# Kernel tuning notes

Hardware: AMD Instinct MI355X
Metric: run time of the kernel (lower is better)

## Reference

```python
import jax, jax.numpy as jnp
import numpy as np

B, IN, OUT = 131072, 128, 32
GRID_SIZE, SPLINE_ORDER = 5, 3
GRID_LO, GRID_HI = -1.0, 1.0
N_BASIS = GRID_SIZE + SPLINE_ORDER  # 8


def _centers_and_spacing():
    n_knots = GRID_SIZE + 2 * SPLINE_ORDER + 1  # 12
    grid = jnp.linspace(GRID_LO, GRID_HI, n_knots)
    centers = grid[SPLINE_ORDER:SPLINE_ORDER + N_BASIS]  # (8,)
    spacing = (GRID_HI - GRID_LO) / GRID_SIZE + 1e-06
    return centers, spacing


def setup_inputs() -> dict:
    key = jax.random.key(0)
    k1, k2, k3 = jax.random.split(key, 3)
    x = jax.random.normal(k1, (B, IN), dtype=jnp.float32)
    coeff = jax.random.normal(k2, (IN, OUT, N_BASIS), dtype=jnp.float32) * 0.1
    base_weight = jnp.ones((IN, OUT), dtype=jnp.float32)
    base_bias = jnp.zeros((IN, OUT), dtype=jnp.float32)
    edge_weights = jax.random.normal(k3, (IN, OUT), dtype=jnp.float32) * 0.1
    return {"x": x, "coeff": coeff, "base_weight": base_weight,
            "base_bias": base_bias, "edge_weights": edge_weights}


def reference(x, coeff, base_weight, base_bias, edge_weights):
    # y[b,j] = sum_i w[i,j] * ( bw[i,j]*silu(x[b,i]) + bb[i,j]
    #                           + sum_k basis[b,i,k]*coeff[i,j,k] )
    centers, spacing = _centers_and_spacing()
    silu = x * jax.nn.sigmoid(x)                                    # (B, I)
    z = (x[:, :, None] - centers[None, None, :]) / spacing          # (B, I, K)
    basis = jnp.exp(-0.5 * z * z)                                   # (B, I, K)
    # base activation contribution
    base_out = jnp.einsum('bi,ij->bj', silu, edge_weights * base_weight)
    bias_out = jnp.sum(edge_weights * base_bias, axis=0)            # (J,)
    # spline contribution: contract over input dim i and basis dim k
    spline_out = jnp.einsum('bik,ijk->bj', basis,
                            edge_weights[:, :, None] * coeff)
    return base_out + bias_out[None, :] + spline_out
```

## Files before the change

### kernel.cpp

```cpp
#include <hip/hip_runtime.h>

typedef short bf16x8 __attribute__((ext_vector_type(8)));
typedef float f32x4v __attribute__((ext_vector_type(4)));

constexpr double H_D    = 0.4 + 1e-6;
constexpr double INVH_D = 1.0 / H_D;
constexpr double C0_D   = -1.0 + 6.0 / 11.0;
constexpr double DLT_D  = (2.0 / 11.0) / H_D;
constexpr double L2E_D  = 1.4426950408889634;

constexpr float INVH = (float)INVH_D;
constexpr float NC0H = (float)(-C0_D * INVH_D);
constexpr float A2f  = (float)(-0.5 * L2E_D);
constexpr float B2f  = (float)(DLT_D * L2E_D);
constexpr float GCF  = (float)(-0.5 * DLT_D * DLT_D * L2E_D);
constexpr float NL2E = (float)(-L2E_D);

__device__ __forceinline__ float fexp2(float v) {
#if __has_builtin(__builtin_amdgcn_exp2f)
  return __builtin_amdgcn_exp2f(v);
#else
  return exp2f(v);
#endif
}
__device__ __forceinline__ float frcp(float v) {
#if __has_builtin(__builtin_amdgcn_rcpf)
  return __builtin_amdgcn_rcpf(v);
#else
  return 1.0f / v;
#endif
}
__device__ __forceinline__ float siluf(float v) {
  return v * frcp(1.0f + fexp2(NL2E * v));
}
__device__ __forceinline__ unsigned pk2(float lo, float hi) {
  unsigned a = __float_as_uint(hi) + 0x8000u;
  unsigned b = __float_as_uint(lo) + 0x8000u;
  return __builtin_amdgcn_perm(a, b, 0x07060302u);
}
__device__ __forceinline__ bf16x8 packfrag(const float (&v)[8]) {
  uint4 d;
  d.x = pk2(v[0], v[1]);
  d.y = pk2(v[2], v[3]);
  d.z = pk2(v[4], v[5]);
  d.w = pk2(v[6], v[7]);
  return __builtin_bit_cast(bf16x8, d);
}
__device__ __forceinline__ unsigned rne16(float f) {
  unsigned u = __float_as_uint(f);
  return (u + 0x7fffu + ((u >> 16) & 1u)) >> 16;
}

__global__ void kan_prep(const float* __restrict__ coeff,
                         const float* __restrict__ bw,
                         const float* __restrict__ bb,
                         const float* __restrict__ ew,
                         uint4* __restrict__ wfrag,
                         float* __restrict__ bias) {
  if (blockIdx.x == 18) {
    __shared__ float part[256];
    const int n = threadIdx.x & 31;
    const int c = threadIdx.x >> 5;
    float s = 0.f;
#pragma unroll
    for (int i = c * 16; i < c * 16 + 16; ++i)
      s += ew[i * 32 + n] * bb[i * 32 + n];
    part[threadIdx.x] = s;
    __syncthreads();
    if (threadIdx.x < 32) {
      float t = 0.f;
#pragma unroll
      for (int c2 = 0; c2 < 8; ++c2) t += part[c2 * 32 + threadIdx.x];
      bias[threadIdx.x] = t;
    }
    return;
  }
  const int e    = blockIdx.x * 4 + (threadIdx.x >> 6);
  const int lane = threadIdx.x & 63;
  const int s = e >> 1, h = e & 1;
  const int G = s / 9, t = s % 9;
  const int n = h * 16 + (lane & 15);
  const int cbase = G * 32 + (lane >> 4) * 8;
  float v[8];
  if (t == 0) {
#pragma unroll
    for (int j = 0; j < 8; ++j) {
      int i = cbase + j;
      v[j] = ew[i * 32 + n] * bw[i * 32 + n];
    }
  } else {
    const int k = t - 1;
    const float g = exp2f(GCF * (float)(k * k));
#pragma unroll
    for (int j = 0; j < 8; ++j) {
      int i = cbase + j;
      v[j] = ew[i * 32 + n] * coeff[(i * 32 + n) * 8 + k] * g;
    }
  }
  uint4 d;
  d.x = (rne16(v[1]) << 16) | rne16(v[0]);
  d.y = (rne16(v[3]) << 16) | rne16(v[2]);
  d.z = (rne16(v[5]) << 16) | rne16(v[4]);
  d.w = (rne16(v[7]) << 16) | rne16(v[6]);
  wfrag[e * 64 + lane] = d;
}

__device__ __forceinline__ void gl_lds16(const uint4* g, uint4* l) {
  __builtin_amdgcn_global_load_lds(
      (const __attribute__((address_space(1))) void*)g,
      (__attribute__((address_space(3))) void*)l, 16, 0, 0);
}

__global__ __launch_bounds__(256, 8) void kan_main(
    const float* __restrict__ x,
    const uint4* __restrict__ wfrag,
    const float* __restrict__ bias,
    float* __restrict__ out) {
  __shared__ uint4 wlds[1152];
  const int tid  = threadIdx.x;
  const int lane = tid & 63;
  const int wave = tid >> 6;
  const int m    = lane & 15;
  const int quad = lane >> 4;
  const long rowbase = ((long)blockIdx.x * 4 + wave) * 16;

  f32x4v acc0, acc1;
#pragma unroll
  for (int rr = 0; rr < 4; ++rr) { acc0[rr] = 0.f; acc1[rr] = 0.f; }

  const float* xbase = x + (rowbase + m) * 128 + (long)quad * 8;

  float xb[8];
  {
    const float4* p = reinterpret_cast<const float4*>(xbase);
    float4 a = p[0], b = p[1];
    xb[0] = a.x; xb[1] = a.y; xb[2] = a.z; xb[3] = a.w;
    xb[4] = b.x; xb[5] = b.y; xb[6] = b.z; xb[7] = b.w;
  }
  const float bv0 = bias[m];
  const float bv1 = bias[m + 16];

#pragma unroll 1
  for (int G = 0; G < 4; ++G) {
    if (G) __syncthreads();
    const uint4* src = wfrag + (size_t)G * 1152;
#pragma unroll
    for (int i = 0; i < 4; ++i)
      gl_lds16(src + tid + i * 256, &wlds[tid + i * 256]);
    if (tid < 128) gl_lds16(src + 1024 + tid, &wlds[1024 + tid]);
    __syncthreads();

    bf16x8 af0;
    float pg[8], rg[8];
    {
      float sv[8];
#pragma unroll
      for (int j = 0; j < 8; ++j) sv[j] = siluf(xb[j]);
      af0 = packfrag(sv);
#pragma unroll
      for (int j = 0; j < 8; ++j) {
        float u = fmaf(xb[j], INVH, NC0H);
        pg[j] = fexp2(A2f * u * u);
        rg[j] = fexp2(B2f * u);
      }
    }

    if (G < 3) {
      const float4* p = reinterpret_cast<const float4*>(xbase + (G + 1) * 32);
      float4 a = p[0], b = p[1];
      xb[0] = a.x; xb[1] = a.y; xb[2] = a.z; xb[3] = a.w;
      xb[4] = b.x; xb[5] = b.y; xb[6] = b.z; xb[7] = b.w;
    }

    const uint4* wl = wlds + lane;

    acc0 = __builtin_amdgcn_mfma_f32_16x16x32_bf16(
        af0, __builtin_bit_cast(bf16x8, wl[0]), acc0, 0, 0, 0);
    acc1 = __builtin_amdgcn_mfma_f32_16x16x32_bf16(
        af0, __builtin_bit_cast(bf16x8, wl[64]), acc1, 0, 0, 0);

#pragma unroll
    for (int t = 1; t <= 8; ++t) {
      bf16x8 c0 = __builtin_bit_cast(bf16x8, wl[t * 128]);
      bf16x8 c1 = __builtin_bit_cast(bf16x8, wl[t * 128 + 64]);
      bf16x8 af = packfrag(pg);
      acc0 = __builtin_amdgcn_mfma_f32_16x16x32_bf16(af, c0, acc0, 0, 0, 0);
      acc1 = __builtin_amdgcn_mfma_f32_16x16x32_bf16(af, c1, acc1, 0, 0, 0);
      if (t < 8) {
#pragma unroll
        for (int j = 0; j < 8; ++j) pg[j] *= rg[j];
      }
    }
  }

#pragma unroll
  for (int rr = 0; rr < 4; ++rr) {
    long row = rowbase + quad * 4 + rr;
    out[row * 32 + m]      = acc0[rr] + bv0;
    out[row * 32 + m + 16] = acc1[rr] + bv1;
  }
}

extern "C" void kernel_launch(void* const* d_in, const int* in_sizes, int n_in,
                              void* d_out, int out_size, void* d_ws, size_t ws_size,
                              hipStream_t stream) {
  const float* x     = (const float*)d_in[0];
  const float* coeff = (const float*)d_in[1];
  const float* bw    = (const float*)d_in[2];
  const float* bb    = (const float*)d_in[3];
  const float* ew    = (const float*)d_in[4];

  uint4* wfrag = (uint4*)d_ws;
  float* bias  = (float*)((char*)d_ws + 73728);

  kan_prep<<<19, 256, 0, stream>>>(coeff, bw, bb, ew, wfrag, bias);
  kan_main<<<2048, 256, 0, stream>>>(x, wfrag, bias, (float*)d_out);
}
```

Before: 117.6 us.

## Double-buffer weight LDS, process two row tiles per wave, use hardware bf16 pack

Each wave now handles 32 rows instead of 16, so every LDS weight fragment read feeds two MFMAs and the grid is halved. The weight slices are double-buffered in LDS, with the next group's global-to-LDS copy issued before the current group's compute, which removes one barrier-bound load stall per group. The manual bf16 rounding trick is replaced by the v_cvt_pk_bf16_f32 instruction. The cost is higher register and LDS use per block, which is why the launch bound drops to 4 blocks per CU and lowers occupancy.

```diff
diff --git a/kernel.cpp b/kernel.cpp
--- a/kernel.cpp
+++ b/kernel.cpp
@@ -33,17 +33,17 @@
 __device__ __forceinline__ float siluf(float v) {
   return v * frcp(1.0f + fexp2(NL2E * v));
 }
-__device__ __forceinline__ unsigned pk2(float lo, float hi) {
-  unsigned a = __float_as_uint(hi) + 0x8000u;
-  unsigned b = __float_as_uint(lo) + 0x8000u;
-  return __builtin_amdgcn_perm(a, b, 0x07060302u);
+__device__ __forceinline__ unsigned pkbf(float lo, float hi) {
+  unsigned r;
+  asm("v_cvt_pk_bf16_f32 %0, %1, %2" : "=v"(r) : "v"(lo), "v"(hi));
+  return r;
 }
 __device__ __forceinline__ bf16x8 packfrag(const float (&v)[8]) {
   uint4 d;
-  d.x = pk2(v[0], v[1]);
-  d.y = pk2(v[2], v[3]);
-  d.z = pk2(v[4], v[5]);
-  d.w = pk2(v[6], v[7]);
+  d.x = pkbf(v[0], v[1]);
+  d.y = pkbf(v[2], v[3]);
+  d.z = pkbf(v[4], v[5]);
+  d.w = pkbf(v[6], v[7]);
   return __builtin_bit_cast(bf16x8, d);
 }
 __device__ __forceinline__ unsigned rne16(float f) {
@@ -111,93 +111,125 @@
       (__attribute__((address_space(3))) void*)l, 16, 0, 0);
 }
 
-__global__ __launch_bounds__(256, 8) void kan_main(
+__device__ __forceinline__ void ld8(const float* p, float (&v)[8]) {
+  const float4* q = reinterpret_cast<const float4*>(p);
+  float4 a = q[0], b = q[1];
+  v[0] = a.x; v[1] = a.y; v[2] = a.z; v[3] = a.w;
+  v[4] = b.x; v[5] = b.y; v[6] = b.z; v[7] = b.w;
+}
+
+__global__ __launch_bounds__(256, 4) void kan_main(
     const float* __restrict__ x,
     const uint4* __restrict__ wfrag,
     const float* __restrict__ bias,
     float* __restrict__ out) {
-  __shared__ uint4 wlds[1152];
+  __shared__ uint4 wlds[2][1152];
   const int tid  = threadIdx.x;
   const int lane = tid & 63;
   const int wave = tid >> 6;
   const int m    = lane & 15;
   const int quad = lane >> 4;
-  const long rowbase = ((long)blockIdx.x * 4 + wave) * 16;
-
-  f32x4v acc0, acc1;
-#pragma unroll
-  for (int rr = 0; rr < 4; ++rr) { acc0[rr] = 0.f; acc1[rr] = 0.f; }
-
-  const float* xbase = x + (rowbase + m) * 128 + (long)quad * 8;
-
-  float xb[8];
-  {
-    const float4* p = reinterpret_cast<const float4*>(xbase);
-    float4 a = p[0], b = p[1];
-    xb[0] = a.x; xb[1] = a.y; xb[2] = a.z; xb[3] = a.w;
-    xb[4] = b.x; xb[5] = b.y; xb[6] = b.z; xb[7] = b.w;
-  }
+  const long rowbase = ((long)blockIdx.x * 4 + wave) * 32;
+
+  f32x4v a0A, a1A, a0B, a1B;
+#pragma unroll
+  for (int rr = 0; rr < 4; ++rr) {
+    a0A[rr] = 0.f; a1A[rr] = 0.f; a0B[rr] = 0.f; a1B[rr] = 0.f;
+  }
+
+  const float* xpA = x + (rowbase + m) * 128 + (long)quad * 8;
+  const float* xpB = xpA + 16 * 128;
+
+  float xa[8], xb[8];
+  ld8(xpA, xa);
+  ld8(xpB, xb);
   const float bv0 = bias[m];
   const float bv1 = bias[m + 16];
 
+  {
+#pragma unroll
+    for (int i = 0; i < 4; ++i)
+      gl_lds16(wfrag + tid + i * 256, &wlds[0][tid + i * 256]);
+    if (tid < 128) gl_lds16(wfrag + 1024 + tid, &wlds[0][1024 + tid]);
+  }
+  __syncthreads();
+
 #pragma unroll 1
   for (int G = 0; G < 4; ++G) {
-    if (G) __syncthreads();
-    const uint4* src = wfrag + (size_t)G * 1152;
-#pragma unroll
-    for (int i = 0; i < 4; ++i)
-      gl_lds16(src + tid + i * 256, &wlds[tid + i * 256]);
-    if (tid < 128) gl_lds16(src + 1024 + tid, &wlds[1024 + tid]);
-    __syncthreads();
-
-    bf16x8 af0;
-    float pg[8], rg[8];
+    if (G < 3) {
+      const uint4* src = wfrag + (size_t)(G + 1) * 1152;
+      uint4* dst = &wlds[(G + 1) & 1][0];
+#pragma unroll
+      for (int i = 0; i < 4; ++i)
+        gl_lds16(src + tid + i * 256, dst + tid + i * 256);
+      if (tid < 128) gl_lds16(src + 1024 + tid, dst + 1024 + tid);
+    }
+
+    bf16x8 sA, sB;
+    float pA[8], rA[8], pB[8], rB[8];
     {
       float sv[8];
 #pragma unroll
+      for (int j = 0; j < 8; ++j) sv[j] = siluf(xa[j]);
+      sA = packfrag(sv);
+#pragma unroll
       for (int j = 0; j < 8; ++j) sv[j] = siluf(xb[j]);
-      af0 = packfrag(sv);
+      sB = packfrag(sv);
+#pragma unroll
+      for (int j = 0; j < 8; ++j) {
+        float u = fmaf(xa[j], INVH, NC0H);
+        pA[j] = fexp2(A2f * u * u);
+        rA[j] = fexp2(B2f * u);
+      }
 #pragma unroll
       for (int j = 0; j < 8; ++j) {
         float u = fmaf(xb[j], INVH, NC0H);
-        pg[j] = fexp2(A2f * u * u);
-        rg[j] = fexp2(B2f * u);
+        pB[j] = fexp2(A2f * u * u);
+        rB[j] = fexp2(B2f * u);
       }
     }
 
     if (G < 3) {
-      const float4* p = reinterpret_cast<const float4*>(xbase + (G + 1) * 32);
-      float4 a = p[0], b = p[1];
-      xb[0] = a.x; xb[1] = a.y; xb[2] = a.z; xb[3] = a.w;
-      xb[4] = b.x; xb[5] = b.y; xb[6] = b.z; xb[7] = b.w;
-    }
-
-    const uint4* wl = wlds + lane;
-
-    acc0 = __builtin_amdgcn_mfma_f32_16x16x32_bf16(
-        af0, __builtin_bit_cast(bf16x8, wl[0]), acc0, 0, 0, 0);
-    acc1 = __builtin_amdgcn_mfma_f32_16x16x32_bf16(
-        af0, __builtin_bit_cast(bf16x8, wl[64]), acc1, 0, 0, 0);
+      ld8(xpA + (G + 1) * 32, xa);
+      ld8(xpB + (G + 1) * 32, xb);
+    }
+
+    const uint4* wl = &wlds[G & 1][0] + lane;
+
+    a0A = __builtin_amdgcn_mfma_f32_16x16x32_bf16(
+        sA, __builtin_bit_cast(bf16x8, wl[0]), a0A, 0, 0, 0);
+    a1A = __builtin_amdgcn_mfma_f32_16x16x32_bf16(
+        sA, __builtin_bit_cast(bf16x8, wl[64]), a1A, 0, 0, 0);
+    a0B = __builtin_amdgcn_mfma_f32_16x16x32_bf16(
+        sB, __builtin_bit_cast(bf16x8, wl[0]), a0B, 0, 0, 0);
+    a1B = __builtin_amdgcn_mfma_f32_16x16x32_bf16(
+        sB, __builtin_bit_cast(bf16x8, wl[64]), a1B, 0, 0, 0);
 
 #pragma unroll
     for (int t = 1; t <= 8; ++t) {
       bf16x8 c0 = __builtin_bit_cast(bf16x8, wl[t * 128]);
       bf16x8 c1 = __builtin_bit_cast(bf16x8, wl[t * 128 + 64]);
-      bf16x8 af = packfrag(pg);
-      acc0 = __builtin_amdgcn_mfma_f32_16x16x32_bf16(af, c0, acc0, 0, 0, 0);
-      acc1 = __builtin_amdgcn_mfma_f32_16x16x32_bf16(af, c1, acc1, 0, 0, 0);
+      bf16x8 fA = packfrag(pA);
+      bf16x8 fB = packfrag(pB);
+      a0A = __builtin_amdgcn_mfma_f32_16x16x32_bf16(fA, c0, a0A, 0, 0, 0);
+      a1A = __builtin_amdgcn_mfma_f32_16x16x32_bf16(fA, c1, a1A, 0, 0, 0);
+      a0B = __builtin_amdgcn_mfma_f32_16x16x32_bf16(fB, c0, a0B, 0, 0, 0);
+      a1B = __builtin_amdgcn_mfma_f32_16x16x32_bf16(fB, c1, a1B, 0, 0, 0);
       if (t < 8) {
 #pragma unroll
-        for (int j = 0; j < 8; ++j) pg[j] *= rg[j];
+        for (int j = 0; j < 8; ++j) { pA[j] *= rA[j]; pB[j] *= rB[j]; }
       }
     }
+    if (G < 3) __syncthreads();
   }
 
 #pragma unroll
   for (int rr = 0; rr < 4; ++rr) {
     long row = rowbase + quad * 4 + rr;
-    out[row * 32 + m]      = acc0[rr] + bv0;
-    out[row * 32 + m + 16] = acc1[rr] + bv1;
+    out[row * 32 + m]             = a0A[rr] + bv0;
+    out[row * 32 + m + 16]        = a1A[rr] + bv1;
+    out[(row + 16) * 32 + m]      = a0B[rr] + bv0;
+    out[(row + 16) * 32 + m + 16] = a1B[rr] + bv1;
   }
 }
 
@@ -214,5 +246,5 @@
   float* bias  = (float*)((char*)d_ws + 73728);
 
   kan_prep<<<19, 256, 0, stream>>>(coeff, bw, bb, ew, wfrag, bias);
-  kan_main<<<2048, 256, 0, stream>>>(x, wfrag, bias, (float*)d_out);
-}
+  kan_main<<<1024, 256, 0, stream>>>(x, wfrag, bias, (float*)d_out);
+}
```

After: 115.1 us. 2.1% less time.
